# Kernel optimization log

Measured on AMD Instinct MI355X. Metric: run time of the kernel, lower is better.

The kernel has to match this reference:

```python
import jax, jax.numpy as jnp
import numpy as np

NUM_HEADS = 8


def setup_inputs() -> dict:
    key = jax.random.key(0)
    B, T, N, C = 16, 24, 716, 256
    H = NUM_HEADS
    D = C // H
    ks = jax.random.split(key, 14)

    def w(k, shape, scale=0.02):
        return jax.random.normal(k, shape, dtype=jnp.float32) * scale

    return {
        "x": jax.random.normal(ks[0], (B, T, N, C), dtype=jnp.float32),
        # nn.Linear weights stored PyTorch-style [out, in]
        "Wq": w(ks[1], (C, C)), "bq": w(ks[2], (C,)),
        "Wk": w(ks[3], (C, C)), "bk": w(ks[4], (C,)),
        "Wv": w(ks[5], (C, C)), "bv": w(ks[6], (C,)),
        "Wo": w(ks[7], (C, C)), "bo": w(ks[8], (C,)),
        # grouped conv1d (kernel_size=1) weights, squeezed: [out_ch, in_ch_per_group]
        "w1": w(ks[9], (C, D)), "b1": w(ks[10], (C,)),
        "w2": w(ks[11], (3 * C, D)), "b2": w(ks[12], (3 * C,)),
    }


def reference(x, Wq, bq, Wk, bk, Wv, bv, Wo, bo, w1, b1, w2, b2):
    B, T, N, C = x.shape
    H = NUM_HEADS
    D = C // H
    BT = B * T
    scale = D ** -0.5

    xf = x.reshape(BT, N, C)
    # q, k, v: [BT, H, N, D]
    q = (xf @ Wq.T + bq).reshape(BT, N, H, D).transpose(0, 2, 1, 3)
    k = (xf @ Wk.T + bk).reshape(BT, N, H, D).transpose(0, 2, 1, 3)
    v = (xf @ Wv.T + bv).reshape(BT, N, H, D).transpose(0, 2, 1, 3)

    # linear attention: kv outer-product [BT, H, D, D], scaled by (scale/N)
    kv = jnp.einsum('bhnd,bhne->bhde', k, v) * (scale / N)
    attn = jnp.einsum('bhnd,bhde->bhne', q, kv)
    # mean-pooled correction term
    kmean = k.mean(axis=2)  # [BT, H, D]
    vmean = v.mean(axis=2)  # [BT, H, D]
    qk = jnp.einsum('bhnd,bhd->bhn', q, kmean) * scale  # [BT, H, N]
    xa = attn + (1.0 - qk)[..., None] * vmean[:, :, None, :]
    xa = xa.transpose(0, 2, 1, 3).reshape(BT, N, C)

    # dynamic per-channel 3-tap kernel weights from node-mean features
    m = xf.mean(axis=1).reshape(BT, H, D)  # grouped input [BT, H, D]
    h1 = jnp.einsum('bgi,goi->bgo', m, w1.reshape(H, D, D)) + b1.reshape(H, D)
    h1 = jax.nn.gelu(h1, approximate=False)
    h2 = jnp.einsum('bgi,goi->bgo', h1, w2.reshape(H, 3 * D, D)) + b2.reshape(H, 3 * D)
    rw = h2.reshape(BT, C, 3)  # per-(sample, channel) 3-tap kernel

    # depthwise conv1d over node axis with groups = BT*C (cross-correlation)
    vc = v.transpose(0, 1, 3, 2).reshape(BT, C, N)
    vp = jnp.pad(vc, ((0, 0), (0, 0), (1, 1)))
    res = (rw[:, :, 0:1] * vp[:, :, 0:N]
           + rw[:, :, 1:2] * vp[:, :, 1:N + 1]
           + rw[:, :, 2:3] * vp[:, :, 2:N + 2])  # [BT, C, N]

    out = (xa + res.transpose(0, 2, 1)).reshape(B, T, N, C)
    return out @ Wo.T + bo
```

## Files before the change

kernel.cpp:

```cpp
#include <hip/hip_runtime.h>
#include <hip/hip_bf16.h>
#include <math.h>

typedef __attribute__((ext_vector_type(8))) short short8;
typedef __attribute__((ext_vector_type(4))) short sv4;
typedef __attribute__((ext_vector_type(4))) float f32x4;
typedef unsigned int u32;

#define BT_ 384
#define N_ 716
#define C_ 256
#define H_ 8
#define D_ 32
#define MROWS (BT_ * N_)
#define SCALE_ 0.17677669529663687f
#define INVN_ (1.0f / 716.0f)

__device__ __forceinline__ void gload_lds16(const void* g, void* l) {
    __builtin_amdgcn_global_load_lds(
        (const __attribute__((address_space(1))) u32*)g,
        (__attribute__((address_space(3))) u32*)l, 16, 0, 0);
}

__global__ void prep_weights(const float* __restrict__ Wq, const float* __restrict__ bq,
                             const float* __restrict__ Wk, const float* __restrict__ bk,
                             const float* __restrict__ Wv, const float* __restrict__ bv,
                             const float* __restrict__ Wo,
                             __hip_bfloat16* __restrict__ wqkv, float* __restrict__ bqkv,
                             __hip_bfloat16* __restrict__ wo) {
    int idx = blockIdx.x * 256 + threadIdx.x;
    if (idx < 768 * 256) {
        int o = idx >> 8, c = idx & 255;
        const float* W = (o < 256) ? Wq : ((o < 512) ? Wk : Wv);
        int oo = o & 255;
        wqkv[idx] = __float2bfloat16(W[oo * 256 + c]);
    }
    if (idx < 256 * 256) wo[idx] = __float2bfloat16(Wo[idx]);
    if (idx < 768) bqkv[idx] = (idx < 256) ? bq[idx] : ((idx < 512) ? bk[idx - 256] : bv[idx - 512]);
}

__global__ __launch_bounds__(256)
void convert_x(const float* __restrict__ x, __hip_bfloat16* __restrict__ xb,
               float* __restrict__ msum) {
    int bt = blockIdx.x, chunk = blockIdx.y;
    int t = threadIdx.x;
    int c4 = (t & 63) * 4;
    int r0 = t >> 6;
    size_t base = ((size_t)bt * N_ + (size_t)chunk * 179) * C_;
    float s0 = 0.f, s1 = 0.f, s2 = 0.f, s3 = 0.f;
    for (int r = r0; r < 179; r += 4) {
        float4 f = *(const float4*)&x[base + (size_t)r * C_ + c4];
        union { sv4 v; __hip_bfloat16 h[4]; } u;
        u.h[0] = __float2bfloat16(f.x);
        u.h[1] = __float2bfloat16(f.y);
        u.h[2] = __float2bfloat16(f.z);
        u.h[3] = __float2bfloat16(f.w);
        *(sv4*)&xb[base + (size_t)r * C_ + c4] = u.v;
        s0 += f.x; s1 += f.y; s2 += f.z; s3 += f.w;
    }
    atomicAdd(&msum[bt * C_ + c4 + 0], s0);
    atomicAdd(&msum[bt * C_ + c4 + 1], s1);
    atomicAdd(&msum[bt * C_ + c4 + 2], s2);
    atomicAdd(&msum[bt * C_ + c4 + 3], s3);
}

__global__ __launch_bounds__(256)
void mlp_rw(const float* __restrict__ msum, const float* __restrict__ w1,
            const float* __restrict__ b1, const float* __restrict__ w2,
            const float* __restrict__ b2, float* __restrict__ rw) {
    int bt = blockIdx.x;
    int t = threadIdx.x;
    __shared__ float m_l[256];
    __shared__ float h1_l[256];
    m_l[t] = msum[bt * 256 + t] * INVN_;
    __syncthreads();
    int g = t >> 5;
    float a = b1[t];
    #pragma unroll
    for (int i = 0; i < 32; ++i) a += m_l[g * 32 + i] * w1[t * 32 + i];
    h1_l[t] = 0.5f * a * (1.0f + erff(a * 0.70710678118654752f));
    __syncthreads();
    for (int o = t; o < 768; o += 256) {
        int gg = o / 96;
        float s = b2[o];
        #pragma unroll
        for (int i = 0; i < 32; ++i) s += h1_l[gg * 32 + i] * w2[o * 32 + i];
        rw[bt * 768 + o] = s;
    }
}

template<int NCOLS, int GRIDX, bool OUT_BF16>
__global__ __launch_bounds__(256, 2)
void gemm_persist(const __hip_bfloat16* __restrict__ A, const __hip_bfloat16* __restrict__ Bm,
                  const float* __restrict__ bias, void* __restrict__ outp) {
    __shared__ __align__(16) __hip_bfloat16 As[2][64 * 256];
    constexpr int NT = MROWS / 64;
    const int L = blockIdx.x;
    const int xcd = L & 7, w = L >> 3;
    const int cb = w % GRIDX;
    const int ib = xcd * 32 + w / GRIDX;
    const int tid = threadIdx.x;
    const int lane = tid & 63;
    const int wave = tid >> 6;
    const int wn = wave;
    const int colBase = cb * 128;
    const int l15 = lane & 15, lq = lane >> 4;
    const int lrow2 = lane >> 5;
    const int p = lane & 31;

    auto stageA = [&](int rt, int buf) {
        #pragma unroll
        for (int i = 0; i < 8; ++i) {
            int r = wave * 16 + 2 * i + lrow2;
            const __hip_bfloat16* g = A + ((size_t)rt * 64 + r) * 256 + ((p ^ (r & 7)) * 8);
            gload_lds16(g, &As[buf][(wave * 16 + 2 * i) * 256]);
        }
    };

    stageA(ib, 0);

    short8 bf[2][8];
    #pragma unroll
    for (int n = 0; n < 2; ++n)
        #pragma unroll
        for (int ks = 0; ks < 8; ++ks)
            bf[n][ks] = *(const short8*)&Bm[(size_t)(colBase + wn * 32 + n * 16 + l15) * 256 + ks * 32 + lq * 8];
    float biasr[2];
    #pragma unroll
    for (int n = 0; n < 2; ++n)
        biasr[n] = bias[colBase + wn * 32 + n * 16 + l15];

    asm volatile("s_waitcnt vmcnt(0)" ::: "memory");
    __builtin_amdgcn_s_barrier();

    int buf = 0;
    for (int rt = ib; rt < NT; rt += 256) {
        int rtn = rt + 256;
        if (rtn < NT) stageA(rtn, buf ^ 1);

        f32x4 acc[4][2] = {};
        #pragma unroll
        for (int ks = 0; ks < 8; ++ks) {
            short8 af[4];
            #pragma unroll
            for (int m = 0; m < 4; ++m) {
                int row = m * 16 + l15;
                af[m] = *(const short8*)&As[buf][row * 256 + (((ks * 4 + lq) ^ (row & 7)) * 8)];
            }
            #pragma unroll
            for (int m = 0; m < 4; ++m)
                #pragma unroll
                for (int n = 0; n < 2; ++n)
                    acc[m][n] = __builtin_amdgcn_mfma_f32_16x16x32_bf16(af[m], bf[n][ks], acc[m][n], 0, 0, 0);
        }
        asm volatile("s_waitcnt lgkmcnt(0)" ::: "memory");
        __builtin_amdgcn_s_barrier();

        if constexpr (OUT_BF16) {
            __hip_bfloat16* Cs = &As[buf][0];
            #pragma unroll
            for (int m = 0; m < 4; ++m)
                #pragma unroll
                for (int n = 0; n < 2; ++n) {
                    int col = wn * 32 + n * 16 + l15;
                    #pragma unroll
                    for (int j = 0; j < 4; ++j)
                        Cs[(m * 16 + lq * 4 + j) * 136 + col] =
                            __float2bfloat16(acc[m][n][j] + biasr[n]);
                }
            asm volatile("s_waitcnt lgkmcnt(0)" ::: "memory");
            __builtin_amdgcn_s_barrier();
            int row = tid >> 2, cq = tid & 3;
            __hip_bfloat16* og = (__hip_bfloat16*)outp + ((size_t)rt * 64 + row) * NCOLS + colBase;
            #pragma unroll
            for (int i = 0; i < 4; ++i) {
                int col = cq * 8 + i * 32;
                *(short8*)&og[col] = *(const short8*)&Cs[row * 136 + col];
            }
        } else {
            float* Cs = (float*)&As[buf][0];
            #pragma unroll
            for (int pp = 0; pp < 2; ++pp) {
                #pragma unroll
                for (int mm = 0; mm < 2; ++mm) {
                    int m = 2 * pp + mm;
                    #pragma unroll
                    for (int n = 0; n < 2; ++n) {
                        int col = wn * 32 + n * 16 + l15;
                        #pragma unroll
                        for (int j = 0; j < 4; ++j)
                            Cs[(mm * 16 + lq * 4 + j) * 132 + col] = acc[m][n][j] + biasr[n];
                    }
                }
                asm volatile("s_waitcnt lgkmcnt(0)" ::: "memory");
                __builtin_amdgcn_s_barrier();
                int row = tid >> 3, k = tid & 7;
                float* og = (float*)outp + ((size_t)rt * 64 + pp * 32 + row) * NCOLS + colBase;
                #pragma unroll
                for (int i = 0; i < 4; ++i) {
                    int col = k * 4 + i * 32;
                    *(float4*)&og[col] = *(const float4*)&Cs[row * 132 + col];
                }
                asm volatile("s_waitcnt lgkmcnt(0)" ::: "memory");
                __builtin_amdgcn_s_barrier();
            }
        }
        asm volatile("s_waitcnt vmcnt(4) lgkmcnt(0)" ::: "memory");
        __builtin_amdgcn_s_barrier();
        buf ^= 1;
    }
}

__global__ __launch_bounds__(512, 2)
void reduce_kv(const __hip_bfloat16* __restrict__ qkv, __hip_bfloat16* __restrict__ kv2t,
               float* __restrict__ vmeanb) {
    __shared__ __align__(16) __hip_bfloat16 T[512 * 64];
    const int bt = blockIdx.x;
    const int tid = threadIdx.x;
    const int lane = tid & 63;
    const int h = tid >> 6;
    const int l15 = lane & 15, lq = lane >> 4;
    const int co = tid >> 3;
    const int np3 = tid & 7;
    const size_t rowbase = (size_t)bt * N_;

    union S8 { short8 v; unsigned short u[8]; };
    const short8 zero8 = {0, 0, 0, 0, 0, 0, 0, 0};

    auto issue_loads = [&](int n0, S8* A, S8* B) {
        #pragma unroll
        for (int s = 0; s < 4; ++s) {
            int n = n0 + 2 * (np3 + 8 * s);
            A[s].v = (n < N_)     ? *(const short8*)&qkv[(rowbase + n) * 768 + 256 + co * 8] : zero8;
            B[s].v = (n + 1 < N_) ? *(const short8*)&qkv[(rowbase + n + 1) * 768 + 256 + co * 8] : zero8;
        }
    };
    auto write_lds = [&](S8* A, S8* B) {
        #pragma unroll
        for (int s = 0; s < 4; ++s) {
            int r = 2 * (np3 + 8 * s);
            int slotbase = ((r >> 3));
            #pragma unroll
            for (int j = 0; j < 8; ++j) {
                int c = co * 8 + j;
                u32 w = (u32)A[s].u[j] | ((u32)B[s].u[j] << 16);
                int off = c * 64 + ((slotbase ^ (c & 7)) << 3) + (r & 7);
                *(u32*)&T[off] = w;
            }
        }
    };

    S8 bufA[4], bufB[4], nxtA[4], nxtB[4];
    issue_loads(0, bufA, bufB);

    f32x4 acc[2][2] = {};
    f32x4 acck[2] = {};
    f32x4 accv[2] = {};
    S8 ones;
    #pragma unroll
    for (int j = 0; j < 8; ++j) ones.u[j] = 0x3F80;

    for (int chunk = 0; chunk < 12; ++chunk) {
        if (chunk < 11) issue_loads((chunk + 1) * 64, nxtA, nxtB);
        write_lds(bufA, bufB);
        __syncthreads();
        #pragma unroll
        for (int nc = 0; nc < 2; ++nc) {
            short8 af[2], bf[2];
            int slot = nc * 4 + lq;
            #pragma unroll
            for (int dh = 0; dh < 2; ++dh) {
                int c = h * 32 + dh * 16 + l15;
                af[dh] = *(const short8*)&T[c * 64 + ((slot ^ (c & 7)) << 3)];
            }
            #pragma unroll
            for (int eh = 0; eh < 2; ++eh) {
                int c = 256 + h * 32 + eh * 16 + l15;
                bf[eh] = *(const short8*)&T[c * 64 + ((slot ^ (c & 7)) << 3)];
            }
            #pragma unroll
            for (int dh = 0; dh < 2; ++dh)
                #pragma unroll
                for (int eh = 0; eh < 2; ++eh)
                    acc[dh][eh] = __builtin_amdgcn_mfma_f32_16x16x32_bf16(af[dh], bf[eh], acc[dh][eh], 0, 0, 0);
            #pragma unroll
            for (int dh = 0; dh < 2; ++dh)
                acck[dh] = __builtin_amdgcn_mfma_f32_16x16x32_bf16(af[dh], ones.v, acck[dh], 0, 0, 0);
            #pragma unroll
            for (int eh = 0; eh < 2; ++eh)
                accv[eh] = __builtin_amdgcn_mfma_f32_16x16x32_bf16(ones.v, bf[eh], accv[eh], 0, 0, 0);
        }
        __syncthreads();
        #pragma unroll
        for (int s = 0; s < 4; ++s) { bufA[s] = nxtA[s]; bufB[s] = nxtB[s]; }
    }

    const int bh = bt * 8 + h;
    #pragma unroll
    for (int eh = 0; eh < 2; ++eh) {
        int e = eh * 16 + l15;
        float vme = accv[eh][0] * INVN_;
        #pragma unroll
        for (int dh = 0; dh < 2; ++dh) {
            union { sv4 v; __hip_bfloat16 x[4]; } o;
            #pragma unroll
            for (int j = 0; j < 4; ++j) {
                float km = acck[dh][j] * INVN_;
                float val = acc[dh][eh][j] * (SCALE_ * INVN_) - SCALE_ * km * vme;
                o.x[j] = __float2bfloat16(val);
            }
            *(sv4*)&kv2t[(size_t)bh * 1024 + e * 32 + dh * 16 + lq * 4] = o.v;
        }
        if (lq == 0) vmeanb[bh * 32 + e] = vme;
    }
}

__global__ __launch_bounds__(256)
void fuse_z2(const __hip_bfloat16* __restrict__ qkv, const __hip_bfloat16* __restrict__ kv2t,
             const float* __restrict__ vmeanb, const float* __restrict__ rw,
             __hip_bfloat16* __restrict__ Z) {
    __shared__ __align__(16) __hip_bfloat16 attn[64][256];
    __shared__ __align__(16) __hip_bfloat16 kvl[8192];
    int bt = blockIdx.x;
    int n0 = blockIdx.y * 64;
    int rows = (N_ - n0 < 64) ? (N_ - n0) : 64;
    int t = threadIdx.x;
    const size_t rowbase = (size_t)bt * N_;

    {
        const __hip_bfloat16* src = kv2t + (size_t)bt * 8192;
        #pragma unroll
        for (int i = 0; i < 4; ++i) {
            int off = (t + i * 256) * 8;
            *(short8*)&kvl[off] = *(const short8*)&src[off];
        }
    }
    __syncthreads();

    {
        int lane = t & 63, wave = t >> 6;
        int l15 = lane & 15, lq = lane >> 4;
        int r0 = wave * 16;
        int gn = n0 + r0 + l15; if (gn > N_ - 1) gn = N_ - 1;
        const __hip_bfloat16* qrow = qkv + (rowbase + gn) * 768;
        #pragma unroll
        for (int h = 0; h < 8; ++h) {
            short8 af = *(const short8*)&qrow[h * 32 + lq * 8];
            #pragma unroll
            for (int half = 0; half < 2; ++half) {
                short8 bfr = *(const short8*)&kvl[h * 1024 + (half * 16 + l15) * 32 + lq * 8];
                f32x4 acc = {};
                acc = __builtin_amdgcn_mfma_f32_16x16x32_bf16(af, bfr, acc, 0, 0, 0);
                int col = h * 32 + half * 16 + l15;
                float vm = vmeanb[bt * 256 + col];
                #pragma unroll
                for (int j = 0; j < 4; ++j)
                    attn[r0 + lq * 4 + j][col] = __float2bfloat16(acc[j] + vm);
            }
        }
    }
    __syncthreads();

    {
        int tr = t >> 5;
        int c8 = (t & 31) * 8;
        float w0[8], w1_[8], w2_[8];
        #pragma unroll
        for (int u = 0; u < 8; ++u) {
            w0[u]  = rw[bt * 768 + (c8 + u) * 3 + 0];
            w1_[u] = rw[bt * 768 + (c8 + u) * 3 + 1];
            w2_[u] = rw[bt * 768 + (c8 + u) * 3 + 2];
        }
        int rbeg = tr * 8;
        if (rbeg < rows) {
            int rend = rbeg + 8; if (rend > rows) rend = rows;
            union U8 { short8 v; __hip_bfloat16 h[8]; };
            auto loadv = [&](int gn, float* dst) {
                if (gn >= 0 && gn < N_) {
                    U8 u; u.v = *(const short8*)&qkv[(rowbase + gn) * 768 + 512 + c8];
                    #pragma unroll
                    for (int uu = 0; uu < 8; ++uu) dst[uu] = __bfloat162float(u.h[uu]);
                } else {
                    #pragma unroll
                    for (int uu = 0; uu < 8; ++uu) dst[uu] = 0.0f;
                }
            };
            float vprev[8], vcur[8], vnext[8];
            loadv(n0 + rbeg - 1, vprev);
            loadv(n0 + rbeg, vcur);
            for (int r = rbeg; r < rend; ++r) {
                int gn = n0 + r;
                loadv(gn + 1, vnext);
                U8 at; at.v = *(const short8*)&attn[r][c8];
                U8 zv;
                #pragma unroll
                for (int u = 0; u < 8; ++u) {
                    float s = __bfloat162float(at.h[u]) + w0[u] * vprev[u]
                              + w1_[u] * vcur[u] + w2_[u] * vnext[u];
                    zv.h[u] = __float2bfloat16(s);
                }
                *(short8*)&Z[(rowbase + gn) * 256 + c8] = zv.v;
                #pragma unroll
                for (int u = 0; u < 8; ++u) { vprev[u] = vcur[u]; vcur[u] = vnext[u]; }
            }
        }
    }
}

extern "C" void kernel_launch(void* const* d_in, const int* in_sizes, int n_in,
                              void* d_out, int out_size, void* d_ws, size_t ws_size,
                              hipStream_t stream) {
    (void)in_sizes; (void)n_in; (void)out_size; (void)ws_size;
    const float* x  = (const float*)d_in[0];
    const float* Wq = (const float*)d_in[1];  const float* bq = (const float*)d_in[2];
    const float* Wk = (const float*)d_in[3];  const float* bk = (const float*)d_in[4];
    const float* Wv = (const float*)d_in[5];  const float* bv = (const float*)d_in[6];
    const float* Wo = (const float*)d_in[7];  const float* bo = (const float*)d_in[8];
    const float* w1 = (const float*)d_in[9];  const float* b1 = (const float*)d_in[10];
    const float* w2 = (const float*)d_in[11]; const float* b2 = (const float*)d_in[12];
    float* out = (float*)d_out;

    char* ws = (char*)d_ws;
    size_t off = 0;
    auto take = [&](size_t bytes) -> char* {
        char* p = ws + off;
        off = (off + bytes + 255) & ~(size_t)255;
        return p;
    };

    __hip_bfloat16* qkv   = (__hip_bfloat16*)take((size_t)MROWS * 768 * 2);
    __hip_bfloat16* xb    = (__hip_bfloat16*)take((size_t)MROWS * 256 * 2);
    __hip_bfloat16* Zbuf  = xb;
    __hip_bfloat16* wqkv  = (__hip_bfloat16*)take(768 * 256 * 2);
    __hip_bfloat16* wo    = (__hip_bfloat16*)take(256 * 256 * 2);
    float* bqkv   = (float*)take(768 * 4);
    float* msum   = (float*)take(384 * 256 * 4);
    float* rw     = (float*)take(384 * 768 * 4);
    __hip_bfloat16* kv2t = (__hip_bfloat16*)take((size_t)384 * 8192 * 2);
    float* vmeanb = (float*)take(384 * 256 * 4);

    hipMemsetAsync(msum, 0, 384 * 256 * 4, stream);

    prep_weights<<<768, 256, 0, stream>>>(Wq, bq, Wk, bk, Wv, bv, Wo, wqkv, bqkv, wo);
    convert_x<<<dim3(384, 4), 256, 0, stream>>>(x, xb, msum);
    mlp_rw<<<384, 256, 0, stream>>>(msum, w1, b1, w2, b2, rw);
    gemm_persist<768, 6, true><<<1536, 256, 0, stream>>>(xb, wqkv, bqkv, qkv);
    reduce_kv<<<384, 512, 0, stream>>>(qkv, kv2t, vmeanb);
    fuse_z2<<<dim3(384, 12), 256, 0, stream>>>(qkv, kv2t, vmeanb, rw, Zbuf);
    gemm_persist<256, 2, false><<<512, 256, 0, stream>>>(Zbuf, wo, bo, out);
}
```

Baseline: 543.8 us.

## Fuse fp32-to-bf16 conversion and node-mean sums into the QKV GEMM

```diff
diff --git a/kernel.cpp b/kernel.cpp
--- a/kernel.cpp
+++ b/kernel.cpp
@@ -13,6 +13,7 @@
 #define H_ 8
 #define D_ 32
 #define MROWS (BT_ * N_)
+#define NT_ (MROWS / 64)
 #define SCALE_ 0.17677669529663687f
 #define INVN_ (1.0f / 716.0f)
 
@@ -40,31 +41,6 @@
 }
 
 __global__ __launch_bounds__(256)
-void convert_x(const float* __restrict__ x, __hip_bfloat16* __restrict__ xb,
-               float* __restrict__ msum) {
-    int bt = blockIdx.x, chunk = blockIdx.y;
-    int t = threadIdx.x;
-    int c4 = (t & 63) * 4;
-    int r0 = t >> 6;
-    size_t base = ((size_t)bt * N_ + (size_t)chunk * 179) * C_;
-    float s0 = 0.f, s1 = 0.f, s2 = 0.f, s3 = 0.f;
-    for (int r = r0; r < 179; r += 4) {
-        float4 f = *(const float4*)&x[base + (size_t)r * C_ + c4];
-        union { sv4 v; __hip_bfloat16 h[4]; } u;
-        u.h[0] = __float2bfloat16(f.x);
-        u.h[1] = __float2bfloat16(f.y);
-        u.h[2] = __float2bfloat16(f.z);
-        u.h[3] = __float2bfloat16(f.w);
-        *(sv4*)&xb[base + (size_t)r * C_ + c4] = u.v;
-        s0 += f.x; s1 += f.y; s2 += f.z; s3 += f.w;
-    }
-    atomicAdd(&msum[bt * C_ + c4 + 0], s0);
-    atomicAdd(&msum[bt * C_ + c4 + 1], s1);
-    atomicAdd(&msum[bt * C_ + c4 + 2], s2);
-    atomicAdd(&msum[bt * C_ + c4 + 3], s3);
-}
-
-__global__ __launch_bounds__(256)
 void mlp_rw(const float* __restrict__ msum, const float* __restrict__ w1,
             const float* __restrict__ b1, const float* __restrict__ w2,
             const float* __restrict__ b2, float* __restrict__ rw) {
@@ -89,12 +65,151 @@
     }
 }
 
-template<int NCOLS, int GRIDX, bool OUT_BF16>
 __global__ __launch_bounds__(256, 2)
-void gemm_persist(const __hip_bfloat16* __restrict__ A, const __hip_bfloat16* __restrict__ Bm,
-                  const float* __restrict__ bias, void* __restrict__ outp) {
+void gemm_xfused(const float* __restrict__ X, const __hip_bfloat16* __restrict__ Bm,
+                 const float* __restrict__ bias, __hip_bfloat16* __restrict__ qkv,
+                 float* __restrict__ msum) {
     __shared__ __align__(16) __hip_bfloat16 As[2][64 * 256];
-    constexpr int NT = MROWS / 64;
+    const int L = blockIdx.x;
+    const int xcd = L & 7, w = L >> 3;
+    const int cb = w % 6;
+    const int ib = xcd * 32 + w / 6;
+    const int tid = threadIdx.x;
+    const int lane = tid & 63;
+    const int wave = tid >> 6;
+    const int wn = wave;
+    const int colBase = cb * 128;
+    const int l15 = lane & 15, lq = lane >> 4;
+    const int slot = tid & 31;
+    const int rowg = tid >> 5;
+    const bool domsum = (cb == 0);
+
+    float4 fA[8], fB[8];
+
+    auto loadX = [&](int rt) {
+        #pragma unroll
+        for (int j = 0; j < 8; ++j) {
+            size_t row = (size_t)rt * 64 + rowg + 8 * j;
+            fA[j] = *(const float4*)&X[row * 256 + slot * 8];
+            fB[j] = *(const float4*)&X[row * 256 + slot * 8 + 4];
+        }
+    };
+    auto stageX = [&](int buf, int rt) {
+        float s0[8], s1[8];
+        int bt0 = 0, rb = 64;
+        if (domsum) {
+            int base = rt * 64;
+            bt0 = base / N_;
+            rb = (bt0 + 1) * N_ - base;
+            #pragma unroll
+            for (int jj = 0; jj < 8; ++jj) { s0[jj] = 0.f; s1[jj] = 0.f; }
+        }
+        #pragma unroll
+        for (int j = 0; j < 8; ++j) {
+            int r = rowg + 8 * j;
+            union { short8 v; __hip_bfloat16 h[8]; } u;
+            u.h[0] = __float2bfloat16(fA[j].x); u.h[1] = __float2bfloat16(fA[j].y);
+            u.h[2] = __float2bfloat16(fA[j].z); u.h[3] = __float2bfloat16(fA[j].w);
+            u.h[4] = __float2bfloat16(fB[j].x); u.h[5] = __float2bfloat16(fB[j].y);
+            u.h[6] = __float2bfloat16(fB[j].z); u.h[7] = __float2bfloat16(fB[j].w);
+            *(short8*)&As[buf][r * 256 + ((slot ^ (r & 7)) * 8)] = u.v;
+            if (domsum) {
+                float in0 = (r < rb) ? 1.0f : 0.0f, in1 = 1.0f - in0;
+                s0[0] += fA[j].x * in0; s1[0] += fA[j].x * in1;
+                s0[1] += fA[j].y * in0; s1[1] += fA[j].y * in1;
+                s0[2] += fA[j].z * in0; s1[2] += fA[j].z * in1;
+                s0[3] += fA[j].w * in0; s1[3] += fA[j].w * in1;
+                s0[4] += fB[j].x * in0; s1[4] += fB[j].x * in1;
+                s0[5] += fB[j].y * in0; s1[5] += fB[j].y * in1;
+                s0[6] += fB[j].z * in0; s1[6] += fB[j].z * in1;
+                s0[7] += fB[j].w * in0; s1[7] += fB[j].w * in1;
+            }
+        }
+        if (domsum) {
+            #pragma unroll
+            for (int jj = 0; jj < 8; ++jj)
+                atomicAdd(&msum[bt0 * 256 + slot * 8 + jj], s0[jj]);
+            if (rb < 64) {
+                #pragma unroll
+                for (int jj = 0; jj < 8; ++jj)
+                    atomicAdd(&msum[(bt0 + 1) * 256 + slot * 8 + jj], s1[jj]);
+            }
+        }
+    };
+
+    short8 bf[2][8];
+    #pragma unroll
+    for (int n = 0; n < 2; ++n)
+        #pragma unroll
+        for (int ks = 0; ks < 8; ++ks)
+            bf[n][ks] = *(const short8*)&Bm[(size_t)(colBase + wn * 32 + n * 16 + l15) * 256 + ks * 32 + lq * 8];
+    float biasr[2];
+    #pragma unroll
+    for (int n = 0; n < 2; ++n)
+        biasr[n] = bias[colBase + wn * 32 + n * 16 + l15];
+
+    loadX(ib);
+    stageX(0, ib);
+    if (ib + 256 < NT_) loadX(ib + 256);
+    asm volatile("s_waitcnt lgkmcnt(0)" ::: "memory");
+    __builtin_amdgcn_s_barrier();
+
+    int buf = 0;
+    for (int rt = ib; rt < NT_; rt += 256) {
+        if (rt + 256 < NT_) stageX(buf ^ 1, rt + 256);
+        if (rt + 512 < NT_) loadX(rt + 512);
+
+        f32x4 acc[4][2] = {};
+        #pragma unroll
+        for (int ks = 0; ks < 8; ++ks) {
+            short8 af[4];
+            #pragma unroll
+            for (int m = 0; m < 4; ++m) {
+                int row = m * 16 + l15;
+                af[m] = *(const short8*)&As[buf][row * 256 + (((ks * 4 + lq) ^ (row & 7)) * 8)];
+            }
+            #pragma unroll
+            for (int m = 0; m < 4; ++m)
+                #pragma unroll
+                for (int n = 0; n < 2; ++n)
+                    acc[m][n] = __builtin_amdgcn_mfma_f32_16x16x32_bf16(af[m], bf[n][ks], acc[m][n], 0, 0, 0);
+        }
+        asm volatile("s_waitcnt lgkmcnt(0)" ::: "memory");
+        __builtin_amdgcn_s_barrier();
+
+        __hip_bfloat16* Cs = &As[buf][0];
+        #pragma unroll
+        for (int m = 0; m < 4; ++m)
+            #pragma unroll
+            for (int n = 0; n < 2; ++n) {
+                int col = wn * 32 + n * 16 + l15;
+                #pragma unroll
+                for (int j = 0; j < 4; ++j)
+                    Cs[(m * 16 + lq * 4 + j) * 136 + col] =
+                        __float2bfloat16(acc[m][n][j] + biasr[n]);
+            }
+        asm volatile("s_waitcnt lgkmcnt(0)" ::: "memory");
+        __builtin_amdgcn_s_barrier();
+        {
+            int row = tid >> 2, cq = tid & 3;
+            __hip_bfloat16* og = qkv + ((size_t)rt * 64 + row) * 768 + colBase;
+            #pragma unroll
+            for (int i = 0; i < 4; ++i) {
+                int col = cq * 8 + i * 32;
+                *(short8*)&og[col] = *(const short8*)&Cs[row * 136 + col];
+            }
+        }
+        asm volatile("s_waitcnt lgkmcnt(0)" ::: "memory");
+        __builtin_amdgcn_s_barrier();
+        buf ^= 1;
+    }
+}
+
+__global__ __launch_bounds__(256, 2)
+void gemm_out(const __hip_bfloat16* __restrict__ A, const __hip_bfloat16* __restrict__ Bm,
+              const float* __restrict__ bias, float* __restrict__ outp) {
+    __shared__ __align__(16) __hip_bfloat16 As[2][64 * 256];
+    constexpr int GRIDX = 2, NCOLS = 256;
     const int L = blockIdx.x;
     const int xcd = L & 7, w = L >> 3;
     const int cb = w % GRIDX;
@@ -134,9 +249,9 @@
     __builtin_amdgcn_s_barrier();
 
     int buf = 0;
-    for (int rt = ib; rt < NT; rt += 256) {
+    for (int rt = ib; rt < NT_; rt += 256) {
         int rtn = rt + 256;
-        if (rtn < NT) stageA(rtn, buf ^ 1);
+        if (rtn < NT_) stageA(rtn, buf ^ 1);
 
         f32x4 acc[4][2] = {};
         #pragma unroll
@@ -156,54 +271,31 @@
         asm volatile("s_waitcnt lgkmcnt(0)" ::: "memory");
         __builtin_amdgcn_s_barrier();
 
-        if constexpr (OUT_BF16) {
-            __hip_bfloat16* Cs = &As[buf][0];
-            #pragma unroll
-            for (int m = 0; m < 4; ++m)
+        float* Cs = (float*)&As[buf][0];
+        #pragma unroll
+        for (int pp = 0; pp < 2; ++pp) {
+            #pragma unroll
+            for (int mm = 0; mm < 2; ++mm) {
+                int m = 2 * pp + mm;
                 #pragma unroll
                 for (int n = 0; n < 2; ++n) {
                     int col = wn * 32 + n * 16 + l15;
                     #pragma unroll
                     for (int j = 0; j < 4; ++j)
-                        Cs[(m * 16 + lq * 4 + j) * 136 + col] =
-                            __float2bfloat16(acc[m][n][j] + biasr[n]);
+                        Cs[(mm * 16 + lq * 4 + j) * 132 + col] = acc[m][n][j] + biasr[n];
                 }
+            }
             asm volatile("s_waitcnt lgkmcnt(0)" ::: "memory");
             __builtin_amdgcn_s_barrier();
-            int row = tid >> 2, cq = tid & 3;
-            __hip_bfloat16* og = (__hip_bfloat16*)outp + ((size_t)rt * 64 + row) * NCOLS + colBase;
+            int row = tid >> 3, k = tid & 7;
+            float* og = outp + ((size_t)rt * 64 + pp * 32 + row) * NCOLS + colBase;
             #pragma unroll
             for (int i = 0; i < 4; ++i) {
-                int col = cq * 8 + i * 32;
-                *(short8*)&og[col] = *(const short8*)&Cs[row * 136 + col];
-            }
-        } else {
-            float* Cs = (float*)&As[buf][0];
-            #pragma unroll
-            for (int pp = 0; pp < 2; ++pp) {
-                #pragma unroll
-                for (int mm = 0; mm < 2; ++mm) {
-                    int m = 2 * pp + mm;
-                    #pragma unroll
-                    for (int n = 0; n < 2; ++n) {
-                        int col = wn * 32 + n * 16 + l15;
-                        #pragma unroll
-                        for (int j = 0; j < 4; ++j)
-                            Cs[(mm * 16 + lq * 4 + j) * 132 + col] = acc[m][n][j] + biasr[n];
-                    }
-                }
-                asm volatile("s_waitcnt lgkmcnt(0)" ::: "memory");
-                __builtin_amdgcn_s_barrier();
-                int row = tid >> 3, k = tid & 7;
-                float* og = (float*)outp + ((size_t)rt * 64 + pp * 32 + row) * NCOLS + colBase;
-                #pragma unroll
-                for (int i = 0; i < 4; ++i) {
-                    int col = k * 4 + i * 32;
-                    *(float4*)&og[col] = *(const float4*)&Cs[row * 132 + col];
-                }
-                asm volatile("s_waitcnt lgkmcnt(0)" ::: "memory");
-                __builtin_amdgcn_s_barrier();
-            }
+                int col = k * 4 + i * 32;
+                *(float4*)&og[col] = *(const float4*)&Cs[row * 132 + col];
+            }
+            asm volatile("s_waitcnt lgkmcnt(0)" ::: "memory");
+            __builtin_amdgcn_s_barrier();
         }
         asm volatile("s_waitcnt vmcnt(4) lgkmcnt(0)" ::: "memory");
         __builtin_amdgcn_s_barrier();
@@ -227,15 +319,15 @@
     union S8 { short8 v; unsigned short u[8]; };
     const short8 zero8 = {0, 0, 0, 0, 0, 0, 0, 0};
 
-    auto issue_loads = [&](int n0, S8* A, S8* B) {
+    auto issue_loads = [&](int n0, S8* Aq, S8* Bq) {
         #pragma unroll
         for (int s = 0; s < 4; ++s) {
             int n = n0 + 2 * (np3 + 8 * s);
-            A[s].v = (n < N_)     ? *(const short8*)&qkv[(rowbase + n) * 768 + 256 + co * 8] : zero8;
-            B[s].v = (n + 1 < N_) ? *(const short8*)&qkv[(rowbase + n + 1) * 768 + 256 + co * 8] : zero8;
+            Aq[s].v = (n < N_)     ? *(const short8*)&qkv[(rowbase + n) * 768 + 256 + co * 8] : zero8;
+            Bq[s].v = (n + 1 < N_) ? *(const short8*)&qkv[(rowbase + n + 1) * 768 + 256 + co * 8] : zero8;
         }
     };
-    auto write_lds = [&](S8* A, S8* B) {
+    auto write_lds = [&](S8* Aq, S8* Bq) {
         #pragma unroll
         for (int s = 0; s < 4; ++s) {
             int r = 2 * (np3 + 8 * s);
@@ -243,9 +335,9 @@
             #pragma unroll
             for (int j = 0; j < 8; ++j) {
                 int c = co * 8 + j;
-                u32 w = (u32)A[s].u[j] | ((u32)B[s].u[j] << 16);
+                u32 wv = (u32)Aq[s].u[j] | ((u32)Bq[s].u[j] << 16);
                 int off = c * 64 + ((slotbase ^ (c & 7)) << 3) + (r & 7);
-                *(u32*)&T[off] = w;
+                *(u32*)&T[off] = wv;
             }
         }
     };
@@ -266,7 +358,7 @@
         __syncthreads();
         #pragma unroll
         for (int nc = 0; nc < 2; ++nc) {
-            short8 af[2], bf[2];
+            short8 af[2], bfr[2];
             int slot = nc * 4 + lq;
             #pragma unroll
             for (int dh = 0; dh < 2; ++dh) {
@@ -276,19 +368,19 @@
             #pragma unroll
             for (int eh = 0; eh < 2; ++eh) {
                 int c = 256 + h * 32 + eh * 16 + l15;
-                bf[eh] = *(const short8*)&T[c * 64 + ((slot ^ (c & 7)) << 3)];
+                bfr[eh] = *(const short8*)&T[c * 64 + ((slot ^ (c & 7)) << 3)];
             }
             #pragma unroll
             for (int dh = 0; dh < 2; ++dh)
                 #pragma unroll
                 for (int eh = 0; eh < 2; ++eh)
-                    acc[dh][eh] = __builtin_amdgcn_mfma_f32_16x16x32_bf16(af[dh], bf[eh], acc[dh][eh], 0, 0, 0);
+                    acc[dh][eh] = __builtin_amdgcn_mfma_f32_16x16x32_bf16(af[dh], bfr[eh], acc[dh][eh], 0, 0, 0);
             #pragma unroll
             for (int dh = 0; dh < 2; ++dh)
                 acck[dh] = __builtin_amdgcn_mfma_f32_16x16x32_bf16(af[dh], ones.v, acck[dh], 0, 0, 0);
             #pragma unroll
             for (int eh = 0; eh < 2; ++eh)
-                accv[eh] = __builtin_amdgcn_mfma_f32_16x16x32_bf16(ones.v, bf[eh], accv[eh], 0, 0, 0);
+                accv[eh] = __builtin_amdgcn_mfma_f32_16x16x32_bf16(ones.v, bfr[eh], accv[eh], 0, 0, 0);
         }
         __syncthreads();
         #pragma unroll
@@ -429,8 +521,7 @@
     };
 
     __hip_bfloat16* qkv   = (__hip_bfloat16*)take((size_t)MROWS * 768 * 2);
-    __hip_bfloat16* xb    = (__hip_bfloat16*)take((size_t)MROWS * 256 * 2);
-    __hip_bfloat16* Zbuf  = xb;
+    __hip_bfloat16* Zbuf  = (__hip_bfloat16*)take((size_t)MROWS * 256 * 2);
     __hip_bfloat16* wqkv  = (__hip_bfloat16*)take(768 * 256 * 2);
     __hip_bfloat16* wo    = (__hip_bfloat16*)take(256 * 256 * 2);
     float* bqkv   = (float*)take(768 * 4);
@@ -442,10 +533,9 @@
     hipMemsetAsync(msum, 0, 384 * 256 * 4, stream);
 
     prep_weights<<<768, 256, 0, stream>>>(Wq, bq, Wk, bk, Wv, bv, Wo, wqkv, bqkv, wo);
-    convert_x<<<dim3(384, 4), 256, 0, stream>>>(x, xb, msum);
+    gemm_xfused<<<1536, 256, 0, stream>>>(x, wqkv, bqkv, qkv, msum);
     mlp_rw<<<384, 256, 0, stream>>>(msum, w1, b1, w2, b2, rw);
-    gemm_persist<768, 6, true><<<1536, 256, 0, stream>>>(xb, wqkv, bqkv, qkv);
     reduce_kv<<<384, 512, 0, stream>>>(qkv, kv2t, vmeanb);
     fuse_z2<<<dim3(384, 12), 256, 0, stream>>>(qkv, kv2t, vmeanb, rw, Zbuf);
-    gemm_persist<256, 2, false><<<512, 256, 0, stream>>>(Zbuf, wo, bo, out);
-}
+    gemm_out<<<512, 256, 0, stream>>>(Zbuf, wo, bo, out);
+}
```

Result: slower. 777.4 us (+43.0%).
